# Kernel optimization log

Measured on AMD Instinct MI355X. Metric: run time of the kernel, lower is better.

## Reference

```python
import jax, jax.numpy as jnp
import numpy as np

N = 50000
E = 600000
IN = 128
H = 4
F = 32  # per-head out; concat output = H*F = 128
NEG_SLOPE = 0.2


def setup_inputs() -> dict:
    key = jax.random.key(0)
    k1, k2, k3, k4, k5, k6 = jax.random.split(key, 6)
    x = jax.random.normal(k1, (N, IN), dtype=jnp.float32)
    edge_index = jax.random.randint(k2, (2, E), 0, N, dtype=jnp.int64)
    W = jax.random.normal(k3, (IN, H * F), dtype=jnp.float32) * 0.05
    att_src = jax.random.normal(k4, (H, F), dtype=jnp.float32) * 0.05
    att_dst = jax.random.normal(k5, (H, F), dtype=jnp.float32) * 0.05
    bias = jnp.zeros((H * F,), dtype=jnp.float32)
    return {"x": x, "edge_index": edge_index, "W": W,
            "att_src": att_src, "att_dst": att_dst, "bias": bias}


def reference(x, edge_index, W, att_src, att_dst, bias):
    n = x.shape[0]
    # add self loops (PyG GATConv default)
    loop = jnp.arange(n, dtype=edge_index.dtype)
    src = jnp.concatenate([edge_index[0], loop])
    dst = jnp.concatenate([edge_index[1], loop])

    h = (x @ W).reshape(n, H, F)                      # [N,H,F]
    a_s = jnp.einsum('nhf,hf->nh', h, att_src)        # [N,H]
    a_d = jnp.einsum('nhf,hf->nh', h, att_dst)        # [N,H]

    e = a_s[src] + a_d[dst]                           # [E',H]
    e = jax.nn.leaky_relu(e, NEG_SLOPE)
    # segment softmax over incoming edges of each destination node
    m = jax.ops.segment_max(e, dst, num_segments=n)   # [N,H]
    m = jnp.where(jnp.isfinite(m), m, 0.0)
    ex = jnp.exp(e - m[dst])                          # [E',H]
    denom = jax.ops.segment_sum(ex, dst, num_segments=n)  # [N,H]
    alpha = ex / denom[dst]                           # [E',H]

    msgs = alpha[:, :, None] * h[src]                 # [E',H,F]
    out = jax.ops.segment_sum(msgs, dst, num_segments=n)  # [N,H,F]
    out = out.reshape(n, H * F) + bias
    return jax.nn.relu(out)
```

## Files before the change

kernel.cpp:

```cpp
#include <hip/hip_runtime.h>

#define NEG_SLOPE 0.2f
#define CAP 64
#define NB 256
#define MAXB 4096
#define A_EDGES 2048
#define A_BLOCKS 293
#define GEMM_BLOCKS 391

typedef __attribute__((ext_vector_type(8))) short short8;
typedef __attribute__((ext_vector_type(4))) float f32x4;

__device__ __forceinline__ unsigned short f2bf(float f) {
    union { float f; unsigned int i; } v; v.f = f;
    unsigned int r = v.i + 0x7FFF + ((v.i >> 16) & 1);
    return (unsigned short)(r >> 16);
}
__device__ __forceinline__ float lrelu(float v) {
    return v > 0.f ? v : NEG_SLOPE * v;
}

__global__ void gat_prep(const float* __restrict__ W,
                         const float* __restrict__ att_src,
                         const float* __restrict__ att_dst,
                         unsigned short* __restrict__ wt,
                         int* __restrict__ bcur)
{
    int i = blockIdx.x * blockDim.x + threadIdx.x;
    if (i < NB) bcur[i] = 0;
    if (i >= 144 * 128) return;
    int r = i >> 7, k = i & 127;
    float v = 0.f;
    if (r < 128) {
        v = W[k * 128 + r];
    } else if (r < 136) {
        int hh = (r - 128) & 3;
        const float* att = (r < 132) ? att_src : att_dst;
        float s = 0.f;
        #pragma unroll 8
        for (int f = 0; f < 32; f++)
            s = fmaf(W[k * 128 + hh * 32 + f], att[hh * 32 + f], s);
        v = s;
    }
    wt[i] = f2bf(v);
}

__global__ __launch_bounds__(256, 2) void gat_mega(
    const float* __restrict__ x, const unsigned short* __restrict__ wt,
    const int* __restrict__ ei, unsigned short* __restrict__ hb,
    float* __restrict__ a_s, float* __restrict__ a_d,
    int* __restrict__ bcur, unsigned int* __restrict__ bbuf, int nE, int n)
{
    __shared__ unsigned short wlds[144 * 128];
    const int bid = blockIdx.x;
    if (bid < A_BLOCKS) {
        int* hist  = (int*)wlds;
        int* gbase = hist + NB;
        const int tid = threadIdx.x;
        hist[tid] = 0;
        __syncthreads();

        int base = bid * A_EDGES + tid * 8;
        int sreg[8], dreg[8], rreg[8];
        bool act = (base + 8 <= nE);
        if (act) {
            int4 s0 = ((const int4*)(ei + base))[0];
            int4 s1 = ((const int4*)(ei + base))[1];
            int4 d0 = ((const int4*)(ei + nE + base))[0];
            int4 d1 = ((const int4*)(ei + nE + base))[1];
            sreg[0]=s0.x; sreg[1]=s0.y; sreg[2]=s0.z; sreg[3]=s0.w;
            sreg[4]=s1.x; sreg[5]=s1.y; sreg[6]=s1.z; sreg[7]=s1.w;
            dreg[0]=d0.x; dreg[1]=d0.y; dreg[2]=d0.z; dreg[3]=d0.w;
            dreg[4]=d1.x; dreg[5]=d1.y; dreg[6]=d1.z; dreg[7]=d1.w;
            #pragma unroll
            for (int j = 0; j < 8; j++)
                rreg[j] = atomicAdd(&hist[dreg[j] >> 8], 1);
        }
        __syncthreads();
        {
            int h = hist[tid];
            gbase[tid] = (h > 0) ? atomicAdd(&bcur[tid], h) : 0;
        }
        __syncthreads();
        if (act) {
            #pragma unroll
            for (int j = 0; j < 8; j++) {
                int b = dreg[j] >> 8;
                int idx = gbase[b] + rreg[j];
                if (idx < MAXB)
                    bbuf[(size_t)b * MAXB + idx] =
                        ((unsigned int)dreg[j] << 16) | (unsigned int)sreg[j];
            }
        }
        return;
    }
    const int tid = threadIdx.x;
    #pragma unroll
    for (int j = 0; j < 9; j++) {
        int i = tid + j * 256;
        int row = i >> 4, s = i & 15;
        int sp = s ^ (row & 7);
        *(short8*)(wlds + row * 128 + sp * 8) = *(const short8*)(wt + (size_t)i * 8);
    }
    __syncthreads();

    const int wave = tid >> 6, lane = tid & 63;
    const int quad = lane >> 4, l15 = lane & 15;
    const int xm = l15 & 7;
    const int m0 = (bid - A_BLOCKS) * 128 + wave * 32;
    if (m0 >= n) return;
    const int row0 = m0 + l15;
    const int row1 = min(m0 + 16 + l15, n - 1);

    f32x4 acc0[9], acc1[9];
    #pragma unroll
    for (int t = 0; t < 9; t++) {
        acc0[t] = (f32x4){0.f, 0.f, 0.f, 0.f};
        acc1[t] = (f32x4){0.f, 0.f, 0.f, 0.f};
    }

    const float* xr0 = x + (size_t)row0 * 128 + quad * 8;
    const float* xr1 = x + (size_t)row1 * 128 + quad * 8;
    #pragma unroll
    for (int kk = 0; kk < 4; ++kk) {
        float4 f0 = ((const float4*)(xr0 + kk * 32))[0];
        float4 f1 = ((const float4*)(xr0 + kk * 32))[1];
        float4 g0 = ((const float4*)(xr1 + kk * 32))[0];
        float4 g1 = ((const float4*)(xr1 + kk * 32))[1];
        short8 afrag0, afrag1;
        afrag0[0] = (short)f2bf(f0.x); afrag0[1] = (short)f2bf(f0.y);
        afrag0[2] = (short)f2bf(f0.z); afrag0[3] = (short)f2bf(f0.w);
        afrag0[4] = (short)f2bf(f1.x); afrag0[5] = (short)f2bf(f1.y);
        afrag0[6] = (short)f2bf(f1.z); afrag0[7] = (short)f2bf(f1.w);
        afrag1[0] = (short)f2bf(g0.x); afrag1[1] = (short)f2bf(g0.y);
        afrag1[2] = (short)f2bf(g0.z); afrag1[3] = (short)f2bf(g0.w);
        afrag1[4] = (short)f2bf(g1.x); afrag1[5] = (short)f2bf(g1.y);
        afrag1[6] = (short)f2bf(g1.z); afrag1[7] = (short)f2bf(g1.w);
        const int sl = (kk * 4 + quad);
        #pragma unroll
        for (int t = 0; t < 9; ++t) {
            short8 bfrag = *(const short8*)(wlds + (size_t)(t * 16 + l15) * 128
                                            + ((sl ^ xm) << 3));
            acc0[t] = __builtin_amdgcn_mfma_f32_16x16x32_bf16(afrag0, bfrag, acc0[t], 0, 0, 0);
            acc1[t] = __builtin_amdgcn_mfma_f32_16x16x32_bf16(afrag1, bfrag, acc1[t], 0, 0, 0);
        }
    }

    #pragma unroll
    for (int t = 0; t < 8; ++t)
        #pragma unroll
        for (int r = 0; r < 4; ++r) {
            int orow0 = m0 + quad * 4 + r;
            hb[(size_t)orow0 * 128 + t * 16 + l15] = f2bf(acc0[t][r]);
            int orow1 = orow0 + 16;
            if (orow1 < n)
                hb[(size_t)orow1 * 128 + t * 16 + l15] = f2bf(acc1[t][r]);
        }
    if (l15 < 8) {
        float* dst = (l15 < 4) ? a_s : a_d;
        int hh = l15 & 3;
        #pragma unroll
        for (int r = 0; r < 4; ++r) {
            int orow0 = m0 + quad * 4 + r;
            dst[(size_t)orow0 * 4 + hh] = acc0[8][r];
            int orow1 = orow0 + 16;
            if (orow1 < n)
                dst[(size_t)orow1 * 4 + hh] = acc1[8][r];
        }
    }
}

__global__ __launch_bounds__(1024) void gat_ell_build(
    const int* __restrict__ bcur, const unsigned int* __restrict__ bbuf,
    unsigned short* __restrict__ csr, int* __restrict__ cnt, int n)
{
    __shared__ int lcnt[NB];
    const int b = blockIdx.x, tid = threadIdx.x;
    if (tid < NB) lcnt[tid] = 0;
    __syncthreads();
    int count = min(bcur[b], MAXB);
    int i = tid * 4;
    if (i < count) {
        uint4 u4 = ((const uint4*)(bbuf + (size_t)b * MAXB))[tid];
        unsigned int uu[4] = {u4.x, u4.y, u4.z, u4.w};
        #pragma unroll
        for (int j = 0; j < 4; j++) {
            if (i + j < count) {
                unsigned int u = uu[j];
                int d = (int)(u >> 16);
                int slot = atomicAdd(&lcnt[d & 255], 1);
                if (slot < CAP)
                    csr[(size_t)d * CAP + slot] = (unsigned short)(u & 0xFFFFu);
            }
        }
    }
    __syncthreads();
    if (tid < NB) {
        int d = (b << 8) + tid;
        if (d < n) cnt[d] = lcnt[tid];
    }
}

__global__ __launch_bounds__(256) void gat_accumulate(
    const int* __restrict__ cnt, const unsigned short* __restrict__ csr,
    const float4* __restrict__ a_s4, const float4* __restrict__ a_d4,
    const uint4* __restrict__ h4, const float* __restrict__ bias,
    float* __restrict__ out, int n)
{
    __shared__ float wtab[4][256];
    __shared__ int   stab[4][64];
    int lane = threadIdx.x & 63;
    int wslot = threadIdx.x >> 6;
    int d = blockIdx.x * 4 + wslot;
    if (d >= n) return;

    int deg  = min(cnt[d], CAP - 1);
    int degi = deg + 1;
    int slotv = (lane < deg) ? (int)csr[(size_t)d * CAP + lane] : d;
    stab[wslot][lane] = slotv;

    float4 ad = a_d4[d];
    float4 w4 = {0.f, 0.f, 0.f, 0.f};
    if (lane < degi) {
        float4 as = a_s4[slotv];
        w4.x = __expf(lrelu(as.x + ad.x));
        w4.y = __expf(lrelu(as.y + ad.y));
        w4.z = __expf(lrelu(as.z + ad.z));
        w4.w = __expf(lrelu(as.w + ad.w));
    }
    ((float4*)wtab[wslot])[lane] = w4;

    int quad = lane >> 4, c = lane & 15;
    int head = c >> 2;
    const float* wrow = wtab[wslot];
    const int*   srow = stab[wslot];

    float acc[8] = {0.f,0.f,0.f,0.f,0.f,0.f,0.f,0.f};
    float den = 0.f;

    for (int j = 0; j < degi; j += 16) {
        int je[4]; int sv[4]; uint4 hv[4];
        #pragma unroll
        for (int u = 0; u < 4; u++) {
            je[u] = j + 4 * u + quad;
            sv[u] = srow[je[u]];
        }
        #pragma unroll
        for (int u = 0; u < 4; u++)
            if (je[u] < degi)
                hv[u] = h4[(size_t)sv[u] * 16 + c];
        #pragma unroll
        for (int u = 0; u < 4; u++) {
            if (je[u] < degi) {
                float w = wrow[je[u] * 4 + head];
                union { unsigned int i; float f; } lo, hi;
                #pragma unroll
                for (int k = 0; k < 4; k++) {
                    unsigned int uu = (&hv[u].x)[k];
                    lo.i = uu << 16; hi.i = uu & 0xFFFF0000u;
                    acc[2*k]   = fmaf(w, lo.f, acc[2*k]);
                    acc[2*k+1] = fmaf(w, hi.f, acc[2*k+1]);
                }
                den += w;
            }
        }
    }

    #pragma unroll
    for (int m = 16; m <= 32; m <<= 1) {
        #pragma unroll
        for (int k = 0; k < 8; k++) acc[k] += __shfl_xor(acc[k], m);
        den += __shfl_xor(den, m);
    }

    if (quad == 0) {
        float inv = 1.f / den;
        float4 b0 = ((const float4*)bias)[2*c];
        float4 b1 = ((const float4*)bias)[2*c + 1];
        float4 o0, o1;
        o0.x = fmaxf(acc[0]*inv + b0.x, 0.f); o0.y = fmaxf(acc[1]*inv + b0.y, 0.f);
        o0.z = fmaxf(acc[2]*inv + b0.z, 0.f); o0.w = fmaxf(acc[3]*inv + b0.w, 0.f);
        o1.x = fmaxf(acc[4]*inv + b1.x, 0.f); o1.y = fmaxf(acc[5]*inv + b1.y, 0.f);
        o1.z = fmaxf(acc[6]*inv + b1.z, 0.f); o1.w = fmaxf(acc[7]*inv + b1.w, 0.f);
        ((float4*)out)[(size_t)d * 32 + 2*c]     = o0;
        ((float4*)out)[(size_t)d * 32 + 2*c + 1] = o1;
    }
}

extern "C" void kernel_launch(void* const* d_in, const int* in_sizes, int n_in,
                              void* d_out, int out_size, void* d_ws, size_t ws_size,
                              hipStream_t stream)
{
    const float* x       = (const float*)d_in[0];
    const int*   ei      = (const int*)d_in[1];
    const float* W       = (const float*)d_in[2];
    const float* att_src = (const float*)d_in[3];
    const float* att_dst = (const float*)d_in[4];
    const float* bias    = (const float*)d_in[5];

    const int n  = in_sizes[0] / 128;
    const int nE = in_sizes[1] / 2;

    char* wsb = (char*)d_ws;
    unsigned short* hb  = (unsigned short*)wsb;
    unsigned short* wt  = hb + (size_t)n * 128;
    float* a_s = (float*)(wt + 144 * 128);
    float* a_d = a_s + (size_t)n * 4;
    int*   cnt  = (int*)(a_d + (size_t)n * 4);
    int*   bcur = cnt + n;
    unsigned short* csr = (unsigned short*)(bcur + NB);
    unsigned int*  bbuf = (unsigned int*)(csr + (size_t)n * CAP);
    float* out = (float*)d_out;

    const int nbkt = (n + 255) >> 8;

    gat_prep<<<(144 * 128 + 255) / 256, 256, 0, stream>>>(W, att_src, att_dst,
                                                          wt, bcur);
    gat_mega<<<A_BLOCKS + GEMM_BLOCKS, 256, 0, stream>>>(x, wt, ei, hb, a_s,
                                                         a_d, bcur, bbuf, nE, n);
    gat_ell_build<<<nbkt, 1024, 0, stream>>>(bcur, bbuf, csr, cnt, n);
    gat_accumulate<<<(n + 3) / 4, 256, 0, stream>>>(cnt, csr, (const float4*)a_s,
                                                    (const float4*)a_d,
                                                    (const uint4*)hb, bias, out, n);
}
```

Baseline: 138.6 us.

## Split GEMM across fill and ELL-build kernels to overlap work

The node-feature GEMM is split into two row ranges. The first range runs alongside the edge bucket-fill in one launch, and the second runs alongside the ELL/CSR build in the next launch, with gemm_body factored into a shared device function. The ELL build now uses 256-thread blocks with a strided loop instead of 1024-thread blocks. The aim is to fill idle compute units during the latency-bound scatter phases and shorten the serial chain of launches, at the cost of more LDS per ELL-build block and more complex block-role dispatch.

```diff
diff --git a/kernel.cpp b/kernel.cpp
--- a/kernel.cpp
+++ b/kernel.cpp
@@ -6,7 +6,9 @@
 #define MAXB 4096
 #define A_EDGES 2048
 #define A_BLOCKS 293
-#define GEMM_BLOCKS 391
+#define GEMM_A_BLOCKS 160
+#define GEMM_B_BLOCKS 231
+#define SPLIT_ROW 20480
 
 typedef __attribute__((ext_vector_type(8))) short short8;
 typedef __attribute__((ext_vector_type(4))) float f32x4;
@@ -45,7 +47,88 @@
     wt[i] = f2bf(v);
 }
 
-__global__ __launch_bounds__(256, 2) void gat_mega(
+__device__ __forceinline__ void gemm_body(
+    const float* __restrict__ x, const unsigned short* __restrict__ wt,
+    unsigned short* __restrict__ hb, float* __restrict__ a_s,
+    float* __restrict__ a_d, unsigned short* wlds, int m0_block, int n)
+{
+    const int tid = threadIdx.x;
+    #pragma unroll
+    for (int j = 0; j < 9; j++) {
+        int i = tid + j * 256;
+        int row = i >> 4, s = i & 15;
+        int sp = s ^ (row & 7);
+        *(short8*)(wlds + row * 128 + sp * 8) = *(const short8*)(wt + (size_t)i * 8);
+    }
+    __syncthreads();
+
+    const int wave = tid >> 6, lane = tid & 63;
+    const int quad = lane >> 4, l15 = lane & 15;
+    const int xm = l15 & 7;
+    const int m0 = m0_block + wave * 32;
+    if (m0 >= n) return;
+    const int row0 = m0 + l15;
+    const int row1 = min(m0 + 16 + l15, n - 1);
+
+    f32x4 acc0[9], acc1[9];
+    #pragma unroll
+    for (int t = 0; t < 9; t++) {
+        acc0[t] = (f32x4){0.f, 0.f, 0.f, 0.f};
+        acc1[t] = (f32x4){0.f, 0.f, 0.f, 0.f};
+    }
+
+    const float* xr0 = x + (size_t)row0 * 128 + quad * 8;
+    const float* xr1 = x + (size_t)row1 * 128 + quad * 8;
+    #pragma unroll
+    for (int kk = 0; kk < 4; ++kk) {
+        float4 f0 = ((const float4*)(xr0 + kk * 32))[0];
+        float4 f1 = ((const float4*)(xr0 + kk * 32))[1];
+        float4 g0 = ((const float4*)(xr1 + kk * 32))[0];
+        float4 g1 = ((const float4*)(xr1 + kk * 32))[1];
+        short8 afrag0, afrag1;
+        afrag0[0] = (short)f2bf(f0.x); afrag0[1] = (short)f2bf(f0.y);
+        afrag0[2] = (short)f2bf(f0.z); afrag0[3] = (short)f2bf(f0.w);
+        afrag0[4] = (short)f2bf(f1.x); afrag0[5] = (short)f2bf(f1.y);
+        afrag0[6] = (short)f2bf(f1.z); afrag0[7] = (short)f2bf(f1.w);
+        afrag1[0] = (short)f2bf(g0.x); afrag1[1] = (short)f2bf(g0.y);
+        afrag1[2] = (short)f2bf(g0.z); afrag1[3] = (short)f2bf(g0.w);
+        afrag1[4] = (short)f2bf(g1.x); afrag1[5] = (short)f2bf(g1.y);
+        afrag1[6] = (short)f2bf(g1.z); afrag1[7] = (short)f2bf(g1.w);
+        const int sl = (kk * 4 + quad);
+        #pragma unroll
+        for (int t = 0; t < 9; ++t) {
+            short8 bfrag = *(const short8*)(wlds + (size_t)(t * 16 + l15) * 128
+                                            + ((sl ^ xm) << 3));
+            acc0[t] = __builtin_amdgcn_mfma_f32_16x16x32_bf16(afrag0, bfrag, acc0[t], 0, 0, 0);
+            acc1[t] = __builtin_amdgcn_mfma_f32_16x16x32_bf16(afrag1, bfrag, acc1[t], 0, 0, 0);
+        }
+    }
+
+    #pragma unroll
+    for (int t = 0; t < 8; ++t)
+        #pragma unroll
+        for (int r = 0; r < 4; ++r) {
+            int orow0 = m0 + quad * 4 + r;
+            hb[(size_t)orow0 * 128 + t * 16 + l15] = f2bf(acc0[t][r]);
+            int orow1 = orow0 + 16;
+            if (orow1 < n)
+                hb[(size_t)orow1 * 128 + t * 16 + l15] = f2bf(acc1[t][r]);
+        }
+    if (l15 < 8) {
+        float* dst = (l15 < 4) ? a_s : a_d;
+        int hh = l15 & 3;
+        #pragma unroll
+        for (int r = 0; r < 4; ++r) {
+            int orow0 = m0 + quad * 4 + r;
+            dst[(size_t)orow0 * 4 + hh] = acc0[8][r];
+            int orow1 = orow0 + 16;
+            if (orow1 < n)
+                dst[(size_t)orow1 * 4 + hh] = acc1[8][r];
+        }
+    }
+}
+
+__global__ __launch_bounds__(256, 2) void gat_fill_gemm(
     const float* __restrict__ x, const unsigned short* __restrict__ wt,
     const int* __restrict__ ei, unsigned short* __restrict__ hb,
     float* __restrict__ a_s, float* __restrict__ a_d,
@@ -94,111 +177,44 @@
         }
         return;
     }
-    const int tid = threadIdx.x;
-    #pragma unroll
-    for (int j = 0; j < 9; j++) {
-        int i = tid + j * 256;
-        int row = i >> 4, s = i & 15;
-        int sp = s ^ (row & 7);
-        *(short8*)(wlds + row * 128 + sp * 8) = *(const short8*)(wt + (size_t)i * 8);
-    }
-    __syncthreads();
-
-    const int wave = tid >> 6, lane = tid & 63;
-    const int quad = lane >> 4, l15 = lane & 15;
-    const int xm = l15 & 7;
-    const int m0 = (bid - A_BLOCKS) * 128 + wave * 32;
-    if (m0 >= n) return;
-    const int row0 = m0 + l15;
-    const int row1 = min(m0 + 16 + l15, n - 1);
-
-    f32x4 acc0[9], acc1[9];
-    #pragma unroll
-    for (int t = 0; t < 9; t++) {
-        acc0[t] = (f32x4){0.f, 0.f, 0.f, 0.f};
-        acc1[t] = (f32x4){0.f, 0.f, 0.f, 0.f};
-    }
-
-    const float* xr0 = x + (size_t)row0 * 128 + quad * 8;
-    const float* xr1 = x + (size_t)row1 * 128 + quad * 8;
-    #pragma unroll
-    for (int kk = 0; kk < 4; ++kk) {
-        float4 f0 = ((const float4*)(xr0 + kk * 32))[0];
-        float4 f1 = ((const float4*)(xr0 + kk * 32))[1];
-        float4 g0 = ((const float4*)(xr1 + kk * 32))[0];
-        float4 g1 = ((const float4*)(xr1 + kk * 32))[1];
-        short8 afrag0, afrag1;
-        afrag0[0] = (short)f2bf(f0.x); afrag0[1] = (short)f2bf(f0.y);
-        afrag0[2] = (short)f2bf(f0.z); afrag0[3] = (short)f2bf(f0.w);
-        afrag0[4] = (short)f2bf(f1.x); afrag0[5] = (short)f2bf(f1.y);
-        afrag0[6] = (short)f2bf(f1.z); afrag0[7] = (short)f2bf(f1.w);
-        afrag1[0] = (short)f2bf(g0.x); afrag1[1] = (short)f2bf(g0.y);
-        afrag1[2] = (short)f2bf(g0.z); afrag1[3] = (short)f2bf(g0.w);
-        afrag1[4] = (short)f2bf(g1.x); afrag1[5] = (short)f2bf(g1.y);
-        afrag1[6] = (short)f2bf(g1.z); afrag1[7] = (short)f2bf(g1.w);
-        const int sl = (kk * 4 + quad);
-        #pragma unroll
-        for (int t = 0; t < 9; ++t) {
-            short8 bfrag = *(const short8*)(wlds + (size_t)(t * 16 + l15) * 128
-                                            + ((sl ^ xm) << 3));
-            acc0[t] = __builtin_amdgcn_mfma_f32_16x16x32_bf16(afrag0, bfrag, acc0[t], 0, 0, 0);
-            acc1[t] = __builtin_amdgcn_mfma_f32_16x16x32_bf16(afrag1, bfrag, acc1[t], 0, 0, 0);
-        }
-    }
-
-    #pragma unroll
-    for (int t = 0; t < 8; ++t)
-        #pragma unroll
-        for (int r = 0; r < 4; ++r) {
-            int orow0 = m0 + quad * 4 + r;
-            hb[(size_t)orow0 * 128 + t * 16 + l15] = f2bf(acc0[t][r]);
-            int orow1 = orow0 + 16;
-            if (orow1 < n)
-                hb[(size_t)orow1 * 128 + t * 16 + l15] = f2bf(acc1[t][r]);
-        }
-    if (l15 < 8) {
-        float* dst = (l15 < 4) ? a_s : a_d;
-        int hh = l15 & 3;
-        #pragma unroll
-        for (int r = 0; r < 4; ++r) {
-            int orow0 = m0 + quad * 4 + r;
-            dst[(size_t)orow0 * 4 + hh] = acc0[8][r];
-            int orow1 = orow0 + 16;
-            if (orow1 < n)
-                dst[(size_t)orow1 * 4 + hh] = acc1[8][r];
-        }
-    }
-}
-
-__global__ __launch_bounds__(1024) void gat_ell_build(
+    gemm_body(x, wt, hb, a_s, a_d, wlds, (bid - A_BLOCKS) * 128, n);
+}
+
+__global__ __launch_bounds__(256, 2) void gat_ell_gemm(
+    const float* __restrict__ x, const unsigned short* __restrict__ wt,
     const int* __restrict__ bcur, const unsigned int* __restrict__ bbuf,
-    unsigned short* __restrict__ csr, int* __restrict__ cnt, int n)
-{
-    __shared__ int lcnt[NB];
-    const int b = blockIdx.x, tid = threadIdx.x;
-    if (tid < NB) lcnt[tid] = 0;
-    __syncthreads();
-    int count = min(bcur[b], MAXB);
-    int i = tid * 4;
-    if (i < count) {
-        uint4 u4 = ((const uint4*)(bbuf + (size_t)b * MAXB))[tid];
-        unsigned int uu[4] = {u4.x, u4.y, u4.z, u4.w};
-        #pragma unroll
-        for (int j = 0; j < 4; j++) {
-            if (i + j < count) {
-                unsigned int u = uu[j];
-                int d = (int)(u >> 16);
-                int slot = atomicAdd(&lcnt[d & 255], 1);
-                if (slot < CAP)
-                    csr[(size_t)d * CAP + slot] = (unsigned short)(u & 0xFFFFu);
+    unsigned short* __restrict__ csr, int* __restrict__ cnt,
+    unsigned short* __restrict__ hb, float* __restrict__ a_s,
+    float* __restrict__ a_d, int nbkt, int n)
+{
+    __shared__ unsigned short wlds[144 * 128];
+    const int bid = blockIdx.x;
+    if (bid < nbkt) {
+        int* lcnt = (int*)wlds;
+        const int b = bid, tid = threadIdx.x;
+        lcnt[tid] = 0;
+        __syncthreads();
+        int count = min(bcur[b], MAXB);
+        for (int i4 = tid; i4 * 4 < count; i4 += 256) {
+            uint4 u4 = ((const uint4*)(bbuf + (size_t)b * MAXB))[i4];
+            unsigned int uu[4] = {u4.x, u4.y, u4.z, u4.w};
+            #pragma unroll
+            for (int j = 0; j < 4; j++) {
+                if (i4 * 4 + j < count) {
+                    unsigned int u = uu[j];
+                    int d = (int)(u >> 16);
+                    int slot = atomicAdd(&lcnt[d & 255], 1);
+                    if (slot < CAP)
+                        csr[(size_t)d * CAP + slot] = (unsigned short)(u & 0xFFFFu);
+                }
             }
         }
-    }
-    __syncthreads();
-    if (tid < NB) {
+        __syncthreads();
         int d = (b << 8) + tid;
         if (d < n) cnt[d] = lcnt[tid];
-    }
+        return;
+    }
+    gemm_body(x, wt, hb, a_s, a_d, wlds, SPLIT_ROW + (bid - nbkt) * 128, n);
 }
 
 __global__ __launch_bounds__(256) void gat_accumulate(
@@ -316,9 +332,10 @@
 
     gat_prep<<<(144 * 128 + 255) / 256, 256, 0, stream>>>(W, att_src, att_dst,
                                                           wt, bcur);
-    gat_mega<<<A_BLOCKS + GEMM_BLOCKS, 256, 0, stream>>>(x, wt, ei, hb, a_s,
-                                                         a_d, bcur, bbuf, nE, n);
-    gat_ell_build<<<nbkt, 1024, 0, stream>>>(bcur, bbuf, csr, cnt, n);
+    gat_fill_gemm<<<A_BLOCKS + GEMM_A_BLOCKS, 256, 0, stream>>>(
+        x, wt, ei, hb, a_s, a_d, bcur, bbuf, nE, n);
+    gat_ell_gemm<<<nbkt + GEMM_B_BLOCKS, 256, 0, stream>>>(
+        x, wt, bcur, bbuf, csr, cnt, hb, a_s, a_d, nbkt, n);
     gat_accumulate<<<(n + 3) / 4, 256, 0, stream>>>(cnt, csr, (const float4*)a_s,
                                                     (const float4*)a_d,
                                                     (const uint4*)hb, bias, out, n);
```

Measured after the change: 140.2 us. No clear change (+1.2%).
